# Kernel optimization log

Measured on AMD Instinct MI355X. Metric: run time of the kernel, lower is better.

The kernel has to match this reference:

```python
import jax, jax.numpy as jnp
import numpy as np

TAU = 10.0
N, D = 4096, 8192  # batch, feature dim (D >= N required by the original indexing)
NUM_CLASSES = 100


def setup_inputs() -> dict:
    key = jax.random.key(0)
    k1, k2 = jax.random.split(key)
    embeddings = jax.random.normal(k1, (N, D), dtype=jnp.float32)
    labels = jax.random.randint(k2, (N,), 0, NUM_CLASSES, dtype=jnp.int64)
    return {"embeddings": embeddings, "labels": labels}


def reference(embeddings, labels):
    # Faithful to the original (buggy) torch math:
    # inner_product[i, d] = exp(emb[i, d]**2 / tau)  (trailing singleton dim dropped)
    n = embeddings.shape[0]
    A = jnp.exp(embeddings * embeddings / TAU)          # [N, D]
    # denominator_i = sum_d A[i, d] - A[i, i]
    denom = jnp.sum(A, axis=1) - jnp.diagonal(A)[:n]    # [N]
    # numerator terms: exp(A[i, j] / tau) for j in batch indices (j < N <= D)
    B = jnp.exp(A[:, :n] / TAU)                          # [N, N]
    same = labels[:, None] == labels[None, :]            # [N, N]
    mask = same & ~jnp.eye(n, dtype=bool)
    counts = jnp.sum(mask, axis=1).astype(embeddings.dtype)   # misma_clase per i
    suma = jnp.sum(jnp.where(mask, B, jnp.zeros((), B.dtype)), axis=1) / denom  # [N]
    return jnp.sum(jnp.log(suma / counts))
```

## Files before the change

kernel.cpp:

```cpp
#include <hip/hip_runtime.h>

static constexpr int N = 4096;
static constexpr int D = 8192;
static constexpr int BLOCK = 256;


__global__ __launch_bounds__(BLOCK) void supcon_kernel(
    const float* __restrict__ emb,
    const int* __restrict__ labels,
    float* __restrict__ out)
{
    __shared__ int s_lab[N];
    __shared__ float s_red[3][4];
    __shared__ int s_cnt[4];

    const int row = blockIdx.x;
    const int tid = threadIdx.x;

    for (int k = tid; k < N / 4; k += BLOCK)
        reinterpret_cast<int4*>(s_lab)[k] = reinterpret_cast<const int4*>(labels)[k];
    __syncthreads();

    const int lab_i = s_lab[row];
    const float* rowp = emb + (size_t)row * D;

    float denom = 0.f, ssum = 0.f, diag = 0.f;
    int cnt = 0;

    for (int j0 = tid * 4; j0 < N; j0 += BLOCK * 4) {
        float4 x = *reinterpret_cast<const float4*>(rowp + j0);
        int4 lj = reinterpret_cast<const int4*>(s_lab)[j0 >> 2];
        float xs[4] = {x.x, x.y, x.z, x.w};
        int   ls[4] = {lj.x, lj.y, lj.z, lj.w};
        #pragma unroll
        for (int k = 0; k < 4; ++k) {
            float a = __expf(xs[k] * xs[k] * 0.1f);
            denom += a;
            int j = j0 + k;
            float b = __expf(a * 0.1f);
            bool match = (ls[k] == lab_i) && (j != row);
            ssum += match ? b : 0.f;
            cnt  += match ? 1 : 0;
            if (j == row) diag = a;
        }
    }

    for (int j0 = N + tid * 4; j0 < D; j0 += BLOCK * 4) {
        float4 x = *reinterpret_cast<const float4*>(rowp + j0);
        denom += __expf(x.x * x.x * 0.1f);
        denom += __expf(x.y * x.y * 0.1f);
        denom += __expf(x.z * x.z * 0.1f);
        denom += __expf(x.w * x.w * 0.1f);
    }

    float fcnt = (float)cnt;
    #pragma unroll
    for (int off = 32; off > 0; off >>= 1) {
        denom += __shfl_down(denom, off);
        ssum  += __shfl_down(ssum,  off);
        diag  += __shfl_down(diag,  off);
        fcnt  += __shfl_down(fcnt,  off);
    }
    const int wave = tid >> 6;
    const int lane = tid & 63;
    if (lane == 0) {
        s_red[0][wave] = denom;
        s_red[1][wave] = ssum;
        s_red[2][wave] = diag;
        s_cnt[wave]    = (int)fcnt;
    }
    __syncthreads();
    if (tid == 0) {
        float dn = 0.f, sv = 0.f, dg = 0.f; int c = 0;
        #pragma unroll
        for (int w = 0; w < 4; ++w) {
            dn += s_red[0][w]; sv += s_red[1][w]; dg += s_red[2][w]; c += s_cnt[w];
        }
        dn -= dg;
        float val = __logf(sv) - __logf(dn) - __logf((float)c);
        atomicAdd(out, val);
    }
}

extern "C" void kernel_launch(void* const* d_in, const int* in_sizes, int n_in,
                              void* d_out, int out_size, void* d_ws, size_t ws_size,
                              hipStream_t stream) {
    const float* emb   = (const float*)d_in[0];
    const int* labels  = (const int*)d_in[1];
    float* out         = (float*)d_out;

    hipMemsetAsync(out, 0, sizeof(float), stream);
    supcon_kernel<<<dim3(N), dim3(BLOCK), 0, stream>>>(emb, labels, out);
}
```

Baseline: 218.7 us.

## Preload row and labels into registers, replace atomic with two-stage reduction

The row kernel now issues all eight float4 loads of a row and four int4 label loads up front into registers, instead of staging labels in shared memory behind a barrier and looping. The single atomicAdd to the output is replaced by writing per-row values to workspace, followed by a second single-block kernel that sums the 4096 values; this also drops the memset. The goal is more memory-level parallelism and less per-block setup and atomic contention, at the cost of higher register pressure and an extra kernel launch.

```diff
diff --git a/kernel.cpp b/kernel.cpp
--- a/kernel.cpp
+++ b/kernel.cpp
@@ -4,56 +4,52 @@
 static constexpr int D = 8192;
 static constexpr int BLOCK = 256;
 
-
-__global__ __launch_bounds__(BLOCK) void supcon_kernel(
+__global__ __launch_bounds__(BLOCK) void supcon_rows(
     const float* __restrict__ emb,
     const int* __restrict__ labels,
-    float* __restrict__ out)
+    float* __restrict__ row_out)
 {
-    __shared__ int s_lab[N];
-    __shared__ float s_red[3][4];
-    __shared__ int s_cnt[4];
-
     const int row = blockIdx.x;
     const int tid = threadIdx.x;
+    const int lab_i = labels[row];
+    const float4* rowp = reinterpret_cast<const float4*>(emb + (size_t)row * D);
+    const int4* labp = reinterpret_cast<const int4*>(labels);
 
-    for (int k = tid; k < N / 4; k += BLOCK)
-        reinterpret_cast<int4*>(s_lab)[k] = reinterpret_cast<const int4*>(labels)[k];
-    __syncthreads();
+    float4 v[8];
+    #pragma unroll
+    for (int it = 0; it < 8; ++it)
+        v[it] = rowp[tid + it * BLOCK];
+    int4 lj[4];
+    #pragma unroll
+    for (int it = 0; it < 4; ++it)
+        lj[it] = labp[tid + it * BLOCK];
 
-    const int lab_i = s_lab[row];
-    const float* rowp = emb + (size_t)row * D;
+    float denom = 0.f, ssum = 0.f, diag = 0.f, fcnt = 0.f;
 
-    float denom = 0.f, ssum = 0.f, diag = 0.f;
-    int cnt = 0;
-
-    for (int j0 = tid * 4; j0 < N; j0 += BLOCK * 4) {
-        float4 x = *reinterpret_cast<const float4*>(rowp + j0);
-        int4 lj = reinterpret_cast<const int4*>(s_lab)[j0 >> 2];
-        float xs[4] = {x.x, x.y, x.z, x.w};
-        int   ls[4] = {lj.x, lj.y, lj.z, lj.w};
+    #pragma unroll
+    for (int it = 0; it < 4; ++it) {
+        const int j0 = (tid + it * BLOCK) * 4;
+        float xs[4] = {v[it].x, v[it].y, v[it].z, v[it].w};
+        int   ls[4] = {lj[it].x, lj[it].y, lj[it].z, lj[it].w};
         #pragma unroll
         for (int k = 0; k < 4; ++k) {
             float a = __expf(xs[k] * xs[k] * 0.1f);
             denom += a;
-            int j = j0 + k;
             float b = __expf(a * 0.1f);
-            bool match = (ls[k] == lab_i) && (j != row);
+            bool match = (ls[k] == lab_i) && (j0 + k != row);
             ssum += match ? b : 0.f;
-            cnt  += match ? 1 : 0;
-            if (j == row) diag = a;
+            fcnt += match ? 1.f : 0.f;
+            diag += (j0 + k == row) ? a : 0.f;
         }
     }
-
-    for (int j0 = N + tid * 4; j0 < D; j0 += BLOCK * 4) {
-        float4 x = *reinterpret_cast<const float4*>(rowp + j0);
-        denom += __expf(x.x * x.x * 0.1f);
-        denom += __expf(x.y * x.y * 0.1f);
-        denom += __expf(x.z * x.z * 0.1f);
-        denom += __expf(x.w * x.w * 0.1f);
+    #pragma unroll
+    for (int it = 4; it < 8; ++it) {
+        float xs[4] = {v[it].x, v[it].y, v[it].z, v[it].w};
+        #pragma unroll
+        for (int k = 0; k < 4; ++k)
+            denom += __expf(xs[k] * xs[k] * 0.1f);
     }
 
-    float fcnt = (float)cnt;
     #pragma unroll
     for (int off = 32; off > 0; off >>= 1) {
         denom += __shfl_down(denom, off);
@@ -61,34 +57,55 @@
         diag  += __shfl_down(diag,  off);
         fcnt  += __shfl_down(fcnt,  off);
     }
+
+    __shared__ float s_red[4][4];
     const int wave = tid >> 6;
-    const int lane = tid & 63;
-    if (lane == 0) {
+    if ((tid & 63) == 0) {
         s_red[0][wave] = denom;
         s_red[1][wave] = ssum;
         s_red[2][wave] = diag;
-        s_cnt[wave]    = (int)fcnt;
+        s_red[3][wave] = fcnt;
     }
     __syncthreads();
     if (tid == 0) {
-        float dn = 0.f, sv = 0.f, dg = 0.f; int c = 0;
+        float dn = 0.f, sv = 0.f, dg = 0.f, c = 0.f;
         #pragma unroll
         for (int w = 0; w < 4; ++w) {
-            dn += s_red[0][w]; sv += s_red[1][w]; dg += s_red[2][w]; c += s_cnt[w];
+            dn += s_red[0][w]; sv += s_red[1][w]; dg += s_red[2][w]; c += s_red[3][w];
         }
         dn -= dg;
-        float val = __logf(sv) - __logf(dn) - __logf((float)c);
-        atomicAdd(out, val);
+        row_out[row] = __logf(sv) - __logf(dn) - __logf(c);
+    }
+}
+
+__global__ __launch_bounds__(1024) void reduce_rows(
+    const float* __restrict__ row_vals, float* __restrict__ out)
+{
+    const int tid = threadIdx.x;
+    float4 x = reinterpret_cast<const float4*>(row_vals)[tid];
+    float s = x.x + x.y + x.z + x.w;
+    #pragma unroll
+    for (int off = 32; off > 0; off >>= 1)
+        s += __shfl_down(s, off);
+    __shared__ float sb[16];
+    if ((tid & 63) == 0) sb[tid >> 6] = s;
+    __syncthreads();
+    if (tid == 0) {
+        float t = 0.f;
+        #pragma unroll
+        for (int w = 0; w < 16; ++w) t += sb[w];
+        *out = t;
     }
 }
 
 extern "C" void kernel_launch(void* const* d_in, const int* in_sizes, int n_in,
                               void* d_out, int out_size, void* d_ws, size_t ws_size,
                               hipStream_t stream) {
-    const float* emb   = (const float*)d_in[0];
-    const int* labels  = (const int*)d_in[1];
-    float* out         = (float*)d_out;
+    const float* emb  = (const float*)d_in[0];
+    const int* labels = (const int*)d_in[1];
+    float* out        = (float*)d_out;
+    float* row_vals   = (float*)d_ws;
 
-    hipMemsetAsync(out, 0, sizeof(float), stream);
-    supcon_kernel<<<dim3(N), dim3(BLOCK), 0, stream>>>(emb, labels, out);
+    supcon_rows<<<dim3(N), dim3(BLOCK), 0, stream>>>(emb, labels, row_vals);
+    reduce_rows<<<dim3(1), dim3(1024), 0, stream>>>(row_vals, out);
 }
```

Result: faster. 187.8 us (-14.1%).
